# Optimization experiments

Measured on AMD Instinct MI355X. Metric: run time of the kernel, lower is better.

The kernel has to match this reference:

```python
import jax, jax.numpy as jnp
import numpy as np

IN_FEATURES = 1024
OUT_FEATURES = 1024
THRESHOLD = 0.05


def ternary_quantize(x, threshold):
    # {-1, 0, +1}: zero where |x| < threshold, else sign(x)
    return jnp.where(jnp.abs(x) < threshold, jnp.zeros_like(x), jnp.sign(x))


def setup_inputs() -> dict:
    key = jax.random.key(0)
    kx, kw = jax.random.split(key)
    x = jax.random.normal(kx, (32768, IN_FEATURES), dtype=jnp.float32)
    # xavier_uniform for weight [out, in]: bound = sqrt(6/(fan_in+fan_out))
    bound = float(np.sqrt(6.0 / (IN_FEATURES + OUT_FEATURES)))
    weight = jax.random.uniform(kw, (OUT_FEATURES, IN_FEATURES), dtype=jnp.float32,
                                minval=-bound, maxval=bound)
    return {"x": x, "weight": weight}


def reference(x, weight):
    x_tern = ternary_quantize(x, THRESHOLD).astype(jnp.int8)
    w_tern = ternary_quantize(weight, THRESHOLD).astype(jnp.int8)
    # int32 accumulate matmul: [T, in] @ [in, out] -> [T, out]
    out = jnp.matmul(x_tern.astype(jnp.int32), w_tern.astype(jnp.int32).T)
    return out.astype(jnp.float32)
```

## Files before the change

### kernel.cpp

```cpp
#include <hip/hip_runtime.h>

#define THRESH 0.05f

typedef __attribute__((ext_vector_type(4))) int   int32x4;
typedef __attribute__((ext_vector_type(4))) float floatx4;

__global__ __launch_bounds__(256) void quant_w_kernel(const float* __restrict__ w,
                                                      signed char* __restrict__ wqf) {
    int c = blockIdx.x * 256 + threadIdx.x;
    int l15  = c & 15;
    int quad = (c >> 4) & 3;
    int nb   = (c >> 6) & 63;
    int kb   = c >> 12;
    int col   = nb * 16 + l15;
    int kbase = kb * 64 + quad * 16;
    const float* src = w + col * 1024 + kbase;
    signed char q[16];
    #pragma unroll
    for (int j = 0; j < 4; ++j) {
        float4 f = *(const float4*)(src + j * 4);
        q[j * 4 + 0] = (signed char)((f.x >= THRESH) - (f.x <= -THRESH));
        q[j * 4 + 1] = (signed char)((f.y >= THRESH) - (f.y <= -THRESH));
        q[j * 4 + 2] = (signed char)((f.z >= THRESH) - (f.z <= -THRESH));
        q[j * 4 + 3] = (signed char)((f.w >= THRESH) - (f.w <= -THRESH));
    }
    *(int32x4*)(wqf + (size_t)c * 16) = *(const int32x4*)q;
}

__global__ __launch_bounds__(256, 4) void tern_gemm_kernel(const float* __restrict__ x,
                                                           const signed char* __restrict__ wqf,
                                                           float* __restrict__ out) {
    __shared__ __attribute__((aligned(16))) signed char a_lds[32 * 1024];
    const int tid = threadIdx.x;
    const long rowbase = (long)blockIdx.x * 32;

    #pragma unroll
    for (int i = 0; i < 8; ++i) {
        int c   = tid + i * 256;
        int row = c >> 6;
        int cir = c & 63;
        const floatx4* src = (const floatx4*)(x + (rowbase + row) * 1024 + cir * 16);
        signed char q[16];
        #pragma unroll
        for (int j = 0; j < 4; ++j) {
            floatx4 f = __builtin_nontemporal_load(src + j);
            #pragma unroll
            for (int e = 0; e < 4; ++e)
                q[j * 4 + e] = (signed char)((f[e] >= THRESH) - (f[e] <= -THRESH));
        }
        int swz = (cir ^ (row & 7)) * 16;
        *(int32x4*)(a_lds + row * 1024 + swz) = *(const int32x4*)q;
    }
    __syncthreads();

    const int wave = tid >> 6;
    const int lane = tid & 63;
    const int l15  = lane & 15;
    const int lq   = lane >> 4;

    for (int colit = 0; colit < 16; ++colit) {
        const int nb = colit * 4 + wave;

        int32x4 bf[16];
        #pragma unroll
        for (int k = 0; k < 16; ++k)
            bf[k] = *(const int32x4*)(wqf + (size_t)(k * 64 + nb) * 1024 + lane * 16);
        __builtin_amdgcn_sched_barrier(0);

        int32x4 acc[2];
        acc[0] = (int32x4){0, 0, 0, 0};
        acc[1] = (int32x4){0, 0, 0, 0};

        #pragma unroll
        for (int k = 0; k < 16; ++k) {
            const int kchunk = k * 4 + lq;
            #pragma unroll
            for (int ri = 0; ri < 2; ++ri) {
                int m = ri * 16 + l15;
                int32x4 af = *(const int32x4*)(a_lds + m * 1024 + ((kchunk ^ (m & 7)) * 16));
                acc[ri] = __builtin_amdgcn_mfma_i32_16x16x64_i8(bf[k], af, acc[ri], 0, 0, 0);
            }
        }

        const int cb = colit * 64 + wave * 16;
        #pragma unroll
        for (int ri = 0; ri < 2; ++ri) {
            const long row = rowbase + ri * 16 + l15;
            floatx4 v;
            v[0] = (float)acc[ri][0];
            v[1] = (float)acc[ri][1];
            v[2] = (float)acc[ri][2];
            v[3] = (float)acc[ri][3];
            __builtin_nontemporal_store(v, (floatx4*)(out + row * 1024 + cb + lq * 4));
        }
    }
}

extern "C" void kernel_launch(void* const* d_in, const int* in_sizes, int n_in,
                              void* d_out, int out_size, void* d_ws, size_t ws_size,
                              hipStream_t stream) {
    const float* x = (const float*)d_in[0];
    const float* w = (const float*)d_in[1];
    float* out = (float*)d_out;
    signed char* wqf = (signed char*)d_ws;

    quant_w_kernel<<<dim3(256), dim3(256), 0, stream>>>(w, wqf);
    tern_gemm_kernel<<<dim3(1024), dim3(256), 0, stream>>>(x, wqf, out);
}
```

Before: 289.1 us.

## Switch ternary GEMM to 32x32x32 int8 MFMA with two accumulator tiles per wave

New measurement: 276.9 us. 1.04x faster.

```diff
diff --git a/kernel.cpp b/kernel.cpp
--- a/kernel.cpp
+++ b/kernel.cpp
@@ -2,18 +2,18 @@
 
 #define THRESH 0.05f
 
-typedef __attribute__((ext_vector_type(4))) int   int32x4;
-typedef __attribute__((ext_vector_type(4))) float floatx4;
+typedef __attribute__((ext_vector_type(4)))  int   int32x4;
+typedef __attribute__((ext_vector_type(16))) int   int32x16;
+typedef __attribute__((ext_vector_type(4)))  float floatx4;
 
 __global__ __launch_bounds__(256) void quant_w_kernel(const float* __restrict__ w,
                                                       signed char* __restrict__ wqf) {
     int c = blockIdx.x * 256 + threadIdx.x;
-    int l15  = c & 15;
-    int quad = (c >> 4) & 3;
-    int nb   = (c >> 6) & 63;
-    int kb   = c >> 12;
-    int col   = nb * 16 + l15;
-    int kbase = kb * 64 + quad * 16;
+    int l  = c & 63;
+    int k  = (c >> 6) & 31;
+    int nb = c >> 11;
+    int col   = nb * 32 + (l & 31);
+    int kbase = k * 32 + (l >> 5) * 16;
     const float* src = w + col * 1024 + kbase;
     signed char q[16];
     #pragma unroll
@@ -53,45 +53,45 @@
     }
     __syncthreads();
 
-    const int wave = tid >> 6;
-    const int lane = tid & 63;
-    const int l15  = lane & 15;
-    const int lq   = lane >> 4;
+    const int wave  = tid >> 6;
+    const int lane  = tid & 63;
+    const int l31   = lane & 31;
+    const int hi    = lane >> 5;
+    const int ex    = l31 & 7;
+    const int abase = l31 * 1024;
 
-    for (int colit = 0; colit < 16; ++colit) {
-        const int nb = colit * 4 + wave;
+    for (int ot = 0; ot < 4; ++ot) {
+        const int nb0 = ot * 8 + wave * 2;
+        const signed char* bp = wqf + (size_t)nb0 * 32768 + lane * 16;
 
-        int32x4 bf[16];
-        #pragma unroll
-        for (int k = 0; k < 16; ++k)
-            bf[k] = *(const int32x4*)(wqf + (size_t)(k * 64 + nb) * 1024 + lane * 16);
-        __builtin_amdgcn_sched_barrier(0);
-
-        int32x4 acc[2];
-        acc[0] = (int32x4){0, 0, 0, 0};
-        acc[1] = (int32x4){0, 0, 0, 0};
+        int32x16 acc0 = {0,0,0,0,0,0,0,0,0,0,0,0,0,0,0,0};
+        int32x16 acc1 = {0,0,0,0,0,0,0,0,0,0,0,0,0,0,0,0};
 
         #pragma unroll
-        for (int k = 0; k < 16; ++k) {
-            const int kchunk = k * 4 + lq;
+        for (int ks = 0; ks < 8; ++ks) {
+            int32x4 b0[4], b1[4];
             #pragma unroll
-            for (int ri = 0; ri < 2; ++ri) {
-                int m = ri * 16 + l15;
-                int32x4 af = *(const int32x4*)(a_lds + m * 1024 + ((kchunk ^ (m & 7)) * 16));
-                acc[ri] = __builtin_amdgcn_mfma_i32_16x16x64_i8(bf[k], af, acc[ri], 0, 0, 0);
+            for (int j = 0; j < 4; ++j) {
+                b0[j] = *(const int32x4*)(bp + (size_t)(ks * 4 + j) * 1024);
+                b1[j] = *(const int32x4*)(bp + 32768 + (size_t)(ks * 4 + j) * 1024);
+            }
+            __builtin_amdgcn_sched_barrier(0);
+            #pragma unroll
+            for (int j = 0; j < 4; ++j) {
+                int k2 = (ks * 4 + j) * 2 + hi;
+                int32x4 af = *(const int32x4*)(a_lds + abase + ((k2 ^ ex) * 16));
+                acc0 = __builtin_amdgcn_mfma_i32_32x32x32_i8(af, b0[j], acc0, 0, 0, 0);
+                acc1 = __builtin_amdgcn_mfma_i32_32x32x32_i8(af, b1[j], acc1, 0, 0, 0);
             }
         }
 
-        const int cb = colit * 64 + wave * 16;
+        const int cb = ot * 256 + wave * 64 + l31;
         #pragma unroll
-        for (int ri = 0; ri < 2; ++ri) {
-            const long row = rowbase + ri * 16 + l15;
-            floatx4 v;
-            v[0] = (float)acc[ri][0];
-            v[1] = (float)acc[ri][1];
-            v[2] = (float)acc[ri][2];
-            v[3] = (float)acc[ri][3];
-            __builtin_nontemporal_store(v, (floatx4*)(out + row * 1024 + cb + lq * 4));
+        for (int r = 0; r < 16; ++r) {
+            int row = (r & 3) + 8 * (r >> 2) + 4 * hi;
+            float* o = out + (rowbase + row) * 1024 + cb;
+            __builtin_nontemporal_store((float)acc0[r], o);
+            __builtin_nontemporal_store((float)acc1[r], o + 32);
         }
     }
 }
```
